# Kernel optimization log

Measured on AMD Instinct MI355X. Metric: run time of the kernel, lower is better.

The kernel has to match this reference:

```python
import jax, jax.numpy as jnp
import numpy as np

HEADS = 16

def setup_inputs() -> dict:
    key = jax.random.key(0)
    k1, k2, k3 = jax.random.split(key, 3)
    b, t, d = 2, 2048, 1024
    x = jax.random.normal(k1, (b, t, d), dtype=jnp.float32)
    w_qkv = jax.random.normal(k2, (d, 3 * d), dtype=jnp.float32) * (d ** -0.5)
    w_out = jax.random.normal(k3, (d, d), dtype=jnp.float32) * (d ** -0.5)
    b_out = jnp.zeros((d,), dtype=jnp.float32)
    return {"x": x, "w_qkv": w_qkv, "w_out": w_out, "b_out": b_out}

def reference(x, w_qkv, w_out, b_out):
    b, t, d = x.shape
    h = HEADS
    dh = d // h
    qkv = x @ w_qkv                      # [b, t, 3d]
    q, k, v = jnp.split(qkv, 3, axis=-1)
    split_heads = lambda a: a.reshape(b, t, h, dh).transpose(0, 2, 1, 3)  # [b,h,t,dh]
    q, k, v = map(split_heads, (q, k, v))
    # NOTE: faithful to source — no 1/sqrt(dh) scaling, causal=False so no mask
    dots = jnp.einsum('bhid,bhjd->bhij', q, k)      # [b,h,t,t]
    attn = jax.nn.softmax(dots, axis=-1)
    out = jnp.einsum('bhjd,bhij->bhid', v, attn)    # [b,h,t,dh]
    out = out.transpose(0, 2, 1, 3).reshape(b, t, d)
    return out @ w_out + b_out
```

## Files before the change

kernel.cpp:

```cpp
#include <hip/hip_runtime.h>
#include <hip/hip_bf16.h>
#include <stdint.h>

typedef __attribute__((ext_vector_type(4))) float f32x4;
typedef __attribute__((ext_vector_type(8))) short bf16x8;

#define MFMA(a, b, c) __builtin_amdgcn_mfma_f32_16x16x32_bf16((a), (b), (c), 0, 0, 0)
#define BAR do { __builtin_amdgcn_s_barrier(); asm volatile("" ::: "memory"); } while (0)

template <int N> __device__ __forceinline__ void waitcnt_vm() {
  if constexpr (N == 0) asm volatile("s_waitcnt vmcnt(0)" ::: "memory");
  else if constexpr (N == 3) asm volatile("s_waitcnt vmcnt(3)" ::: "memory");
  else if constexpr (N == 4) asm volatile("s_waitcnt vmcnt(4)" ::: "memory");
}

__device__ __forceinline__ uint16_t f2b(float f) {
  uint32_t u = __builtin_bit_cast(uint32_t, f);
  uint32_t r = (u + 0x7FFFu + ((u >> 16) & 1u)) >> 16;
  return (uint16_t)r;
}

__device__ __forceinline__ uint32_t cvt_pk_bf16(float lo, float hi) {
  uint32_t r;
  asm("v_cvt_pk_bf16_f32 %0, %1, %2" : "=v"(r) : "v"(lo), "v"(hi));
  return r;
}

__device__ __forceinline__ float fexp2(float x) {
  float r;
  asm("v_exp_f32 %0, %1" : "=v"(r) : "v"(x));
  return r;
}

__device__ __forceinline__ void dot2_acc(float& l, uint32_t p, uint32_t ones2) {
  asm("v_dot2_f32_bf16 %0, %1, %2, %0" : "+v"(l) : "v"(p), "v"(ones2));
}

__device__ __forceinline__ void gld_lds16(const void* g, void* l) {
  __builtin_amdgcn_global_load_lds((const __attribute__((address_space(1))) uint32_t*)g,
                                   (__attribute__((address_space(3))) uint32_t*)l, 16, 0, 0);
}

__device__ __forceinline__ int swz(int r) {
  return (r & 3) | ((((r >> 2) ^ (r >> 3)) & 1) << 2);
}

__global__ __launch_bounds__(256) void prologue(const float* __restrict__ x,
                                                const float* __restrict__ wqkv,
                                                const float* __restrict__ wout,
                                                uint16_t* __restrict__ xb,
                                                uint16_t* __restrict__ wqkvT,
                                                uint16_t* __restrict__ woutT) {
  __shared__ float t_[32][33];
  const int bid = blockIdx.x;
  if (bid < 4096) {
    const int i = (bid * 256 + threadIdx.x) * 4;
    const float4 v = *(const float4*)(x + i);
    ushort4 o;
    o.x = f2b(v.x); o.y = f2b(v.y); o.z = f2b(v.z); o.w = f2b(v.w);
    *(ushort4*)(xb + i) = o;
    return;
  }
  const float* in;
  uint16_t* out;
  int C, bx, by;
  if (bid < 7168) { in = wqkv; out = wqkvT; C = 3072; bx = (bid - 4096) % 96; by = (bid - 4096) / 96; }
  else            { in = wout; out = woutT; C = 1024; bx = (bid - 7168) & 31;  by = (bid - 7168) >> 5; }
  const int R = 1024;
  const int c0 = bx * 32, r0 = by * 32;
  const int tx = threadIdx.x & 31, ty = threadIdx.x >> 5;
#pragma unroll
  for (int i = 0; i < 4; i++)
    t_[ty + i * 8][tx] = in[(size_t)(r0 + ty + i * 8) * C + c0 + tx];
  __syncthreads();
#pragma unroll
  for (int i = 0; i < 4; i++)
    out[(size_t)(c0 + ty + i * 8) * R + r0 + tx] = f2b(t_[tx][ty + i * 8]);
}

template <int NOUT, int BN, bool BF16_OUT, bool BIAS, bool SCALEQ, bool VSPLIT>
__global__ __launch_bounds__(256) void gemm_bt(const uint16_t* __restrict__ A,
                                               const uint16_t* __restrict__ Bt,
                                               const float* __restrict__ bias,
                                               void* __restrict__ Cout,
                                               uint16_t* __restrict__ VTout) {
  constexpr int NF = BN / 32;
  constexpr int TILEB = 8192 + BN * 64;
  constexpr int NL = 2 + BN / 64;
  __shared__ __align__(16) char LDS[3 * TILEB];
  const int tid = threadIdx.x;
  const int wave = tid >> 6, lane = tid & 63;
  const int lr = lane & 15, lg = lane >> 4;

  const int nwg = gridDim.x * gridDim.y;
  const int id0 = blockIdx.y * gridDim.x + blockIdx.x;
  const int sid = (id0 & 7) * (nwg >> 3) + (id0 >> 3);
  const int row0 = (sid / gridDim.x) * 128, col0 = (sid % gridDim.x) * BN;
  const int wr = (wave >> 1) * 64, wc = (wave & 1) * (BN / 2);

  f32x4 acc[4][NF] = {};

  const int ldsOff = wave * 1024 + lane * 16;
  const int srow = ldsOff >> 6;
  const int scolB = (((lane & 3) ^ ((lane >> 3) & 3)) << 4);
  const char* ApA = (const char*)A + ((size_t)(row0 + srow) * 1024) * 2 + scolB;
  const char* ApB = ApA + 64 * 2048;
  const char* BpA = (const char*)Bt + ((size_t)(col0 + srow) * 1024) * 2 + scolB;
  const char* BpB = BpA + 64 * 2048;

  auto stage = [&](int t, char* base) {
    char* d = base + wave * 1024;
    const int kk = t * 64;
    gld_lds16(ApA + kk, d);
    gld_lds16(ApB + kk, d + 4096);
    gld_lds16(BpA + kk, d + 8192);
    if constexpr (BN == 128) gld_lds16(BpB + kk, d + 12288);
  };
  const int csw = ((lr >> 1) & 3);
  const int rcol = (lg ^ csw) * 16;
  auto compute = [&](const char* S) {
    bf16x8 af[4], bfv[NF];
#pragma unroll
    for (int i = 0; i < 4; i++)
      af[i] = *(const bf16x8*)(S + (wr + i * 16 + lr) * 64 + rcol);
#pragma unroll
    for (int j = 0; j < NF; j++)
      bfv[j] = *(const bf16x8*)(S + 8192 + (wc + j * 16 + lr) * 64 + rcol);
    __builtin_amdgcn_s_setprio(1);
#pragma unroll
    for (int i = 0; i < 4; i++)
#pragma unroll
      for (int j = 0; j < NF; j++)
        acc[i][j] = MFMA(af[i], bfv[j], acc[i][j]);
    __builtin_amdgcn_s_setprio(0);
  };

  stage(0, LDS);
  stage(1, LDS + TILEB);
#pragma unroll 1
  for (int i = 0; i < 30; i += 3) {
    waitcnt_vm<NL>(); BAR; stage(i + 2, LDS + 2 * TILEB); compute(LDS);
    waitcnt_vm<NL>(); BAR; stage(i + 3, LDS);             compute(LDS + TILEB);
    waitcnt_vm<NL>(); BAR; stage(i + 4, LDS + TILEB);     compute(LDS + 2 * TILEB);
  }
  waitcnt_vm<NL>(); BAR; compute(LDS);
  waitcnt_vm<0>();  BAR; compute(LDS + TILEB);

  const float qs = (SCALEQ && col0 < 1024) ? 1.4426950408889634f : 1.0f;
#pragma unroll
  for (int i = 0; i < 4; i++)
#pragma unroll
    for (int j = 0; j < NF; j++) {
      const int col = col0 + wc + j * 16 + lr;
      const int rowb = row0 + wr + i * 16 + lg * 4;
      if (VSPLIT && col >= 2048) {
        ushort4 vs;
        vs.x = f2b(acc[i][j][0]); vs.y = f2b(acc[i][j][1]);
        vs.z = f2b(acc[i][j][2]); vs.w = f2b(acc[i][j][3]);
        const int bIdx = rowb >> 11, tok = rowb & 2047;
        *(ushort4*)(VTout + (size_t)(bIdx * 1024 + (col - 2048)) * 2048 + tok) = vs;
      } else {
        const float bv = BIAS ? bias[col] : 0.f;
#pragma unroll
        for (int r = 0; r < 4; r++) {
          const float v = acc[i][j][r] * qs + bv;
          if (BF16_OUT) ((uint16_t*)Cout)[(size_t)(rowb + r) * NOUT + col] = f2b(v);
          else          ((float*)Cout)[(size_t)(rowb + r) * NOUT + col] = v;
        }
      }
    }
}

__global__ __launch_bounds__(256) void attn_fwd(const uint16_t* __restrict__ qkv,
                                                const uint16_t* __restrict__ VT,
                                                uint16_t* __restrict__ O) {
  __shared__ __align__(16) char LDS[4 * 16384];
  const int tid = threadIdx.x;
  const int wave = tid >> 6, lane = tid & 63;
  const int lr = lane & 15, lg = lane >> 4;
  const int id = blockIdx.x;
  const int w = id >> 3;
  const int bh = (id & 7) * 4 + (w >> 4);
  const int qt = w & 15;
  const int b = bh >> 4, h = bh & 15;
  const int q0 = qt * 128 + wave * 32;

  const uint16_t* Qp = qkv + (size_t)(b * 2048 + q0 + lr) * 3072 + h * 64 + lg * 8;
  const bf16x8 qA0 = *(const bf16x8*)Qp;
  const bf16x8 qA1 = *(const bf16x8*)(Qp + 32);
  const bf16x8 qB0 = *(const bf16x8*)(Qp + 16 * 3072);
  const bf16x8 qB1 = *(const bf16x8*)(Qp + 16 * 3072 + 32);

  const int off1 = wave * 1024 + lane * 16;
  const int off2 = off1 + 4096;
  const int r1 = off1 >> 7, c1 = (off1 >> 4) & 7;
  const int r2 = off2 >> 7, c2 = (off2 >> 4) & 7;
  const char* qb = (const char*)qkv;
  const char* vb = (const char*)VT;
  const char* Kp1 = qb + ((size_t)(b * 2048 + r1) * 3072 + 1024 + h * 64) * 2 + (c1 ^ swz(r1)) * 16;
  const char* Kp2 = qb + ((size_t)(b * 2048 + r2) * 3072 + 1024 + h * 64) * 2 + (c2 ^ swz(r2)) * 16;
  const char* Vp1 = vb + ((size_t)(bh * 64 + r1) * 2048) * 2 + (c1 ^ swz(r1)) * 16;
  const char* Vp2 = vb + ((size_t)(bh * 64 + r2) * 2048) * 2 + (c2 ^ swz(r2)) * 16;

  const int wb1 = wave * 1024;
  const int wb2 = 4096 + wave * 1024;

  auto stage = [&](size_t t, char* slot) {
    const size_t ka = t * 393216;
    const int va = (int)t * 128;
    gld_lds16(Kp1 + ka, slot + wb1);
    gld_lds16(Kp2 + ka, slot + wb2);
    gld_lds16(Vp1 + va, slot + 8192 + wb1);
    gld_lds16(Vp2 + va, slot + 8192 + wb2);
  };

  int koff[8], voff[8];
  const int rbase = ((lr >> 2) << 3) | (lr & 3);
#pragma unroll
  for (int fj = 0; fj < 4; fj++) {
    const int row = rbase + ((fj & 1) << 2) + ((fj >> 1) << 5);
    const int sw = swz(row);
    koff[fj * 2]     = row * 128 + ((lg ^ sw) * 16);
    koff[fj * 2 + 1] = row * 128 + (((4 + lg) ^ sw) * 16);
  }
#pragma unroll
  for (int cf = 0; cf < 4; cf++) {
    const int dr = cf * 16 + lr;
    const int sw = swz(dr);
    voff[cf * 2]     = 8192 + dr * 128 + ((lg ^ sw) * 16);
    voff[cf * 2 + 1] = 8192 + dr * 128 + (((4 + lg) ^ sw) * 16);
  }

  f32x4 oA[4] = {}, oB[4] = {};
  float lA0 = 0.f, lA1 = 0.f, lB0 = 0.f, lB1 = 0.f;
  const uint32_t ones2 = 0x3F803F80u;
  const f32x4 z4 = {0.f, 0.f, 0.f, 0.f};
  const char* ldsB = (const char*)LDS;

  union PW { uint32_t u[8]; struct { bf16x8 a0, a1; } f; };

  auto compute = [&](int sb) {
    f32x4 s0[4], s1[4];
    __builtin_amdgcn_s_setprio(1);
#pragma unroll
    for (int fj = 0; fj < 4; fj++) {
      const bf16x8 k0 = *(const bf16x8*)(ldsB + sb + koff[fj * 2]);
      const bf16x8 k1 = *(const bf16x8*)(ldsB + sb + koff[fj * 2 + 1]);
      s0[fj] = MFMA(k0, qA0, z4);
      s0[fj] = MFMA(k1, qA1, s0[fj]);
      s1[fj] = MFMA(k0, qB0, z4);
      s1[fj] = MFMA(k1, qB1, s1[fj]);
    }
    __builtin_amdgcn_s_setprio(0);
    bf16x8 v0[4], v1[4];
#pragma unroll
    for (int cf = 0; cf < 4; cf++) {
      v0[cf] = *(const bf16x8*)(ldsB + sb + voff[cf * 2]);
      v1[cf] = *(const bf16x8*)(ldsB + sb + voff[cf * 2 + 1]);
    }
    PW pA, pB;
#pragma unroll
    for (int fj = 0; fj < 4; fj++) {
      const float a0 = fexp2(s0[fj][0]), a1 = fexp2(s0[fj][1]);
      const float a2 = fexp2(s0[fj][2]), a3 = fexp2(s0[fj][3]);
      pA.u[fj * 2]     = cvt_pk_bf16(a0, a1);
      pA.u[fj * 2 + 1] = cvt_pk_bf16(a2, a3);
      const float b0 = fexp2(s1[fj][0]), b1 = fexp2(s1[fj][1]);
      const float b2 = fexp2(s1[fj][2]), b3 = fexp2(s1[fj][3]);
      pB.u[fj * 2]     = cvt_pk_bf16(b0, b1);
      pB.u[fj * 2 + 1] = cvt_pk_bf16(b2, b3);
    }
#pragma unroll
    for (int j = 0; j < 8; j += 2) {
      dot2_acc(lA0, pA.u[j], ones2);
      dot2_acc(lA1, pA.u[j + 1], ones2);
      dot2_acc(lB0, pB.u[j], ones2);
      dot2_acc(lB1, pB.u[j + 1], ones2);
    }
    __builtin_amdgcn_s_setprio(1);
#pragma unroll
    for (int cf = 0; cf < 4; cf++) {
      oA[cf] = MFMA(pA.f.a0, v0[cf], oA[cf]);
      oA[cf] = MFMA(pA.f.a1, v1[cf], oA[cf]);
      oB[cf] = MFMA(pB.f.a0, v0[cf], oB[cf]);
      oB[cf] = MFMA(pB.f.a1, v1[cf], oB[cf]);
    }
    __builtin_amdgcn_s_setprio(0);
  };

  stage(0, LDS);
  stage(1, LDS + 16384);
#pragma unroll 1
  for (int t = 0; t < 28; t += 4) {
    waitcnt_vm<0>(); BAR;
    stage(t + 2, LDS + 32768);
    stage(t + 3, LDS + 49152);
    compute(0);
    compute(16384);
    waitcnt_vm<0>(); BAR;
    stage(t + 4, LDS);
    stage(t + 5, LDS + 16384);
    compute(32768);
    compute(49152);
  }
  waitcnt_vm<0>(); BAR;
  stage(30, LDS + 32768);
  stage(31, LDS + 49152);
  compute(0);
  compute(16384);
  waitcnt_vm<0>(); BAR;
  compute(32768);
  compute(49152);

  float lA = lA0 + lA1, lB = lB0 + lB1;
  lA += __shfl_xor(lA, 16, 64); lA += __shfl_xor(lA, 32, 64);
  lB += __shfl_xor(lB, 16, 64); lB += __shfl_xor(lB, 32, 64);

  float invA[4], invB[4];
#pragma unroll
  for (int r = 0; r < 4; r++) {
    invA[r] = 1.0f / __shfl(lA, lg * 4 + r, 64);
    invB[r] = 1.0f / __shfl(lB, lg * 4 + r, 64);
  }
#pragma unroll
  for (int cf = 0; cf < 4; cf++)
#pragma unroll
    for (int r = 0; r < 4; r++) {
      const int col = h * 64 + cf * 16 + lr;
      const int rowA = b * 2048 + q0 + lg * 4 + r;
      O[(size_t)rowA * 1024 + col] = f2b(oA[cf][r] * invA[r]);
      O[(size_t)(rowA + 16) * 1024 + col] = f2b(oB[cf][r] * invB[r]);
    }
}

extern "C" void kernel_launch(void* const* d_in, const int* in_sizes, int n_in,
                              void* d_out, int out_size, void* d_ws, size_t ws_size,
                              hipStream_t stream) {
  const float* x    = (const float*)d_in[0];
  const float* wqkv = (const float*)d_in[1];
  const float* wout = (const float*)d_in[2];
  const float* bout = (const float*)d_in[3];

  char* ws = (char*)d_ws;
  uint16_t* woutT   = (uint16_t*)(ws + 0);
  uint16_t* qkvb    = (uint16_t*)(ws + (2ull  << 20));
  uint16_t* VT      = (uint16_t*)(ws + (26ull << 20));
  uint16_t* xb      = (uint16_t*)(ws + (34ull << 20));
  uint16_t* wqkvT   = (uint16_t*)(ws + (42ull << 20));
  uint16_t* attnout = xb;

  prologue<<<dim3(8192), dim3(256), 0, stream>>>(x, wqkv, wout, xb, wqkvT, woutT);

  gemm_bt<3072, 128, true, false, true, true>
      <<<dim3(24, 32), dim3(256), 0, stream>>>(xb, wqkvT, nullptr, qkvb, VT);
  attn_fwd<<<dim3(512), dim3(256), 0, stream>>>(qkvb, VT, attnout);
  gemm_bt<1024, 128, false, true, false, false>
      <<<dim3(8, 32), dim3(256), 0, stream>>>(attnout, woutT, bout, d_out, nullptr);
}
```

Before: 102.8 us.

## Process 64 query rows per wave in attention to double K/V reuse

Each wave now handles 64 query rows (four 16-row MFMA groups) instead of 32, so every K/V tile staged in LDS feeds twice as many MFMAs. The grid is halved to 256 blocks and launch bounds set to one block per SIMD group. This cuts global and LDS traffic per unit of compute, but raises register pressure and leaves fewer blocks than the 256 CUs to hide latency with.

```diff
diff --git a/kernel.cpp b/kernel.cpp
--- a/kernel.cpp
+++ b/kernel.cpp
@@ -171,25 +171,29 @@
     }
 }
 
-__global__ __launch_bounds__(256) void attn_fwd(const uint16_t* __restrict__ qkv,
-                                                const uint16_t* __restrict__ VT,
-                                                uint16_t* __restrict__ O) {
+__global__ __launch_bounds__(256, 1) void attn_fwd(const uint16_t* __restrict__ qkv,
+                                                   const uint16_t* __restrict__ VT,
+                                                   uint16_t* __restrict__ O) {
   __shared__ __align__(16) char LDS[4 * 16384];
   const int tid = threadIdx.x;
   const int wave = tid >> 6, lane = tid & 63;
   const int lr = lane & 15, lg = lane >> 4;
   const int id = blockIdx.x;
   const int w = id >> 3;
-  const int bh = (id & 7) * 4 + (w >> 4);
-  const int qt = w & 15;
+  const int bh = (id & 7) * 4 + (w >> 3);
+  const int qt = w & 7;
   const int b = bh >> 4, h = bh & 15;
-  const int q0 = qt * 128 + wave * 32;
+  const int q0 = qt * 256 + wave * 64;
 
   const uint16_t* Qp = qkv + (size_t)(b * 2048 + q0 + lr) * 3072 + h * 64 + lg * 8;
   const bf16x8 qA0 = *(const bf16x8*)Qp;
   const bf16x8 qA1 = *(const bf16x8*)(Qp + 32);
   const bf16x8 qB0 = *(const bf16x8*)(Qp + 16 * 3072);
   const bf16x8 qB1 = *(const bf16x8*)(Qp + 16 * 3072 + 32);
+  const bf16x8 qC0 = *(const bf16x8*)(Qp + 32 * 3072);
+  const bf16x8 qC1 = *(const bf16x8*)(Qp + 32 * 3072 + 32);
+  const bf16x8 qD0 = *(const bf16x8*)(Qp + 48 * 3072);
+  const bf16x8 qD1 = *(const bf16x8*)(Qp + 48 * 3072 + 32);
 
   const int off1 = wave * 1024 + lane * 16;
   const int off2 = off1 + 4096;
@@ -231,8 +235,9 @@
     voff[cf * 2 + 1] = 8192 + dr * 128 + (((4 + lg) ^ sw) * 16);
   }
 
-  f32x4 oA[4] = {}, oB[4] = {};
+  f32x4 oA[4] = {}, oB[4] = {}, oC[4] = {}, oD[4] = {};
   float lA0 = 0.f, lA1 = 0.f, lB0 = 0.f, lB1 = 0.f;
+  float lC0 = 0.f, lC1 = 0.f, lD0 = 0.f, lD1 = 0.f;
   const uint32_t ones2 = 0x3F803F80u;
   const f32x4 z4 = {0.f, 0.f, 0.f, 0.f};
   const char* ldsB = (const char*)LDS;
@@ -240,16 +245,16 @@
   union PW { uint32_t u[8]; struct { bf16x8 a0, a1; } f; };
 
   auto compute = [&](int sb) {
-    f32x4 s0[4], s1[4];
+    f32x4 sA[4], sB[4], sC[4], sD[4];
     __builtin_amdgcn_s_setprio(1);
 #pragma unroll
     for (int fj = 0; fj < 4; fj++) {
       const bf16x8 k0 = *(const bf16x8*)(ldsB + sb + koff[fj * 2]);
       const bf16x8 k1 = *(const bf16x8*)(ldsB + sb + koff[fj * 2 + 1]);
-      s0[fj] = MFMA(k0, qA0, z4);
-      s0[fj] = MFMA(k1, qA1, s0[fj]);
-      s1[fj] = MFMA(k0, qB0, z4);
-      s1[fj] = MFMA(k1, qB1, s1[fj]);
+      sA[fj] = MFMA(k0, qA0, z4); sA[fj] = MFMA(k1, qA1, sA[fj]);
+      sB[fj] = MFMA(k0, qB0, z4); sB[fj] = MFMA(k1, qB1, sB[fj]);
+      sC[fj] = MFMA(k0, qC0, z4); sC[fj] = MFMA(k1, qC1, sC[fj]);
+      sD[fj] = MFMA(k0, qD0, z4); sD[fj] = MFMA(k1, qD1, sD[fj]);
     }
     __builtin_amdgcn_s_setprio(0);
     bf16x8 v0[4], v1[4];
@@ -258,32 +263,40 @@
       v0[cf] = *(const bf16x8*)(ldsB + sb + voff[cf * 2]);
       v1[cf] = *(const bf16x8*)(ldsB + sb + voff[cf * 2 + 1]);
     }
-    PW pA, pB;
+    PW pA, pB, pC, pD;
 #pragma unroll
     for (int fj = 0; fj < 4; fj++) {
-      const float a0 = fexp2(s0[fj][0]), a1 = fexp2(s0[fj][1]);
-      const float a2 = fexp2(s0[fj][2]), a3 = fexp2(s0[fj][3]);
+      const float a0 = fexp2(sA[fj][0]), a1 = fexp2(sA[fj][1]);
+      const float a2 = fexp2(sA[fj][2]), a3 = fexp2(sA[fj][3]);
       pA.u[fj * 2]     = cvt_pk_bf16(a0, a1);
       pA.u[fj * 2 + 1] = cvt_pk_bf16(a2, a3);
-      const float b0 = fexp2(s1[fj][0]), b1 = fexp2(s1[fj][1]);
-      const float b2 = fexp2(s1[fj][2]), b3 = fexp2(s1[fj][3]);
+      const float b0 = fexp2(sB[fj][0]), b1 = fexp2(sB[fj][1]);
+      const float b2 = fexp2(sB[fj][2]), b3 = fexp2(sB[fj][3]);
       pB.u[fj * 2]     = cvt_pk_bf16(b0, b1);
       pB.u[fj * 2 + 1] = cvt_pk_bf16(b2, b3);
+      const float c0_ = fexp2(sC[fj][0]), c1_ = fexp2(sC[fj][1]);
+      const float c2_ = fexp2(sC[fj][2]), c3_ = fexp2(sC[fj][3]);
+      pC.u[fj * 2]     = cvt_pk_bf16(c0_, c1_);
+      pC.u[fj * 2 + 1] = cvt_pk_bf16(c2_, c3_);
+      const float d0 = fexp2(sD[fj][0]), d1 = fexp2(sD[fj][1]);
+      const float d2 = fexp2(sD[fj][2]), d3 = fexp2(sD[fj][3]);
+      pD.u[fj * 2]     = cvt_pk_bf16(d0, d1);
+      pD.u[fj * 2 + 1] = cvt_pk_bf16(d2, d3);
     }
 #pragma unroll
     for (int j = 0; j < 8; j += 2) {
-      dot2_acc(lA0, pA.u[j], ones2);
-      dot2_acc(lA1, pA.u[j + 1], ones2);
-      dot2_acc(lB0, pB.u[j], ones2);
-      dot2_acc(lB1, pB.u[j + 1], ones2);
+      dot2_acc(lA0, pA.u[j], ones2); dot2_acc(lA1, pA.u[j + 1], ones2);
+      dot2_acc(lB0, pB.u[j], ones2); dot2_acc(lB1, pB.u[j + 1], ones2);
+      dot2_acc(lC0, pC.u[j], ones2); dot2_acc(lC1, pC.u[j + 1], ones2);
+      dot2_acc(lD0, pD.u[j], ones2); dot2_acc(lD1, pD.u[j + 1], ones2);
     }
     __builtin_amdgcn_s_setprio(1);
 #pragma unroll
     for (int cf = 0; cf < 4; cf++) {
-      oA[cf] = MFMA(pA.f.a0, v0[cf], oA[cf]);
-      oA[cf] = MFMA(pA.f.a1, v1[cf], oA[cf]);
-      oB[cf] = MFMA(pB.f.a0, v0[cf], oB[cf]);
-      oB[cf] = MFMA(pB.f.a1, v1[cf], oB[cf]);
+      oA[cf] = MFMA(pA.f.a0, v0[cf], oA[cf]); oA[cf] = MFMA(pA.f.a1, v1[cf], oA[cf]);
+      oB[cf] = MFMA(pB.f.a0, v0[cf], oB[cf]); oB[cf] = MFMA(pB.f.a1, v1[cf], oB[cf]);
+      oC[cf] = MFMA(pC.f.a0, v0[cf], oC[cf]); oC[cf] = MFMA(pC.f.a1, v1[cf], oC[cf]);
+      oD[cf] = MFMA(pD.f.a0, v0[cf], oD[cf]); oD[cf] = MFMA(pD.f.a1, v1[cf], oD[cf]);
     }
     __builtin_amdgcn_s_setprio(0);
   };
@@ -312,15 +325,19 @@
   compute(32768);
   compute(49152);
 
-  float lA = lA0 + lA1, lB = lB0 + lB1;
+  float lA = lA0 + lA1, lB = lB0 + lB1, lC = lC0 + lC1, lD = lD0 + lD1;
   lA += __shfl_xor(lA, 16, 64); lA += __shfl_xor(lA, 32, 64);
   lB += __shfl_xor(lB, 16, 64); lB += __shfl_xor(lB, 32, 64);
-
-  float invA[4], invB[4];
+  lC += __shfl_xor(lC, 16, 64); lC += __shfl_xor(lC, 32, 64);
+  lD += __shfl_xor(lD, 16, 64); lD += __shfl_xor(lD, 32, 64);
+
+  float invA[4], invB[4], invC[4], invD[4];
 #pragma unroll
   for (int r = 0; r < 4; r++) {
     invA[r] = 1.0f / __shfl(lA, lg * 4 + r, 64);
     invB[r] = 1.0f / __shfl(lB, lg * 4 + r, 64);
+    invC[r] = 1.0f / __shfl(lC, lg * 4 + r, 64);
+    invD[r] = 1.0f / __shfl(lD, lg * 4 + r, 64);
   }
 #pragma unroll
   for (int cf = 0; cf < 4; cf++)
@@ -330,6 +347,8 @@
       const int rowA = b * 2048 + q0 + lg * 4 + r;
       O[(size_t)rowA * 1024 + col] = f2b(oA[cf][r] * invA[r]);
       O[(size_t)(rowA + 16) * 1024 + col] = f2b(oB[cf][r] * invB[r]);
+      O[(size_t)(rowA + 32) * 1024 + col] = f2b(oC[cf][r] * invC[r]);
+      O[(size_t)(rowA + 48) * 1024 + col] = f2b(oD[cf][r] * invD[r]);
     }
 }
 
@@ -353,7 +372,7 @@
 
   gemm_bt<3072, 128, true, false, true, true>
       <<<dim3(24, 32), dim3(256), 0, stream>>>(xb, wqkvT, nullptr, qkvb, VT);
-  attn_fwd<<<dim3(512), dim3(256), 0, stream>>>(qkvb, VT, attnout);
+  attn_fwd<<<dim3(256), dim3(256), 0, stream>>>(qkvb, VT, attnout);
   gemm_bt<1024, 128, false, true, false, false>
       <<<dim3(8, 32), dim3(256), 0, stream>>>(attnout, woutT, bout, d_out, nullptr);
 }
```

Result: no change. 104.1 us (+1.3%).
